# Performance work log

Hardware: AMD Instinct MI355X
Metric: run time of the kernel (lower is better)

Reference implementation:

```python
import jax, jax.numpy as jnp
import numpy as np
from jax import lax

NUM_STEPS = 32
NUM_CLASSES = 10
HIDDEN = 1024


def setup_inputs() -> dict:
    key = jax.random.key(0)
    ks = jax.random.split(key, 4)
    B, H, W, C = 8, 1024, 2048, 4
    x = jax.random.normal(ks[0], (B, H, W, C), dtype=jnp.float32)
    conv_w = jax.random.normal(ks[1], (C,), dtype=jnp.float32) * 0.5
    conv_b = jnp.zeros((1,), dtype=jnp.float32)
    w1 = jax.random.normal(ks[2], (HIDDEN, W), dtype=jnp.float32) * (1.0 / np.sqrt(W))
    b1 = jnp.zeros((HIDDEN,), dtype=jnp.float32)
    w2 = jax.random.normal(ks[3], (NUM_CLASSES, HIDDEN), dtype=jnp.float32) * (1.0 / np.sqrt(HIDDEN))
    b2 = jnp.zeros((NUM_CLASSES,), dtype=jnp.float32)
    beta1 = jnp.full((1,), 0.95, dtype=jnp.float32)
    thr1 = jnp.ones((1,), dtype=jnp.float32)
    beta2 = jnp.full((1,), 0.95, dtype=jnp.float32)
    thr2 = jnp.ones((1,), dtype=jnp.float32)
    return {"x": x, "conv_w": conv_w, "conv_b": conv_b, "w1": w1, "b1": b1,
            "beta1": beta1, "thr1": thr1, "w2": w2, "b2": b2,
            "beta2": beta2, "thr2": thr2}


def _leaky_scan(inp_t, beta, thr):
    # inp_t: [T, ...]; snntorch Leaky, reset_mechanism='subtract', reset_delay=False
    b = jnp.clip(beta, 0.0, 1.0)

    def step(mem, u):
        mem = b * mem + u
        spk = (mem > thr).astype(u.dtype)   # heaviside spike
        mem = mem - spk * thr               # subtract reset (no delay)
        return mem, spk

    mem0 = jnp.zeros(inp_t.shape[1:], dtype=inp_t.dtype)
    _, spks = lax.scan(step, mem0, inp_t)
    return spks  # [T, ...]


def reference(x, conv_w, conv_b, w1, b1, beta1, thr1, w2, b2, beta2, thr2):
    # x: [B, H, W, 4]; 1x1 conv over 4 antenna channels -> 1 channel
    xf = jnp.einsum('bhwc,c->bhw', x, conv_w) + conv_b[0]       # [B, H, W]
    B, H, W = xf.shape
    G = H // NUM_STEPS
    xr = xf.reshape(B, G, NUM_STEPS, W)                          # [B, G, T, 2048]
    h = jnp.einsum('bgtw,dw->bgtd', xr, w1) + b1                 # [B, G, T, D]
    spks1 = _leaky_scan(jnp.moveaxis(h, 2, 0), beta1, thr1)      # [T, B, G, D]
    s = spks1.sum(axis=0)                                        # [B, G, D]
    h2 = jnp.einsum('bgd,cd->bgc', s, w2) + b2                   # [B, G, C]
    spks2 = _leaky_scan(jnp.moveaxis(h2, 1, 0), beta2, thr2)     # [G, B, C]
    logits = spks2.sum(axis=0)                                   # [B, C]
    return jax.nn.softmax(logits, axis=1)
```

## Files before the change

kernel.cpp:

```cpp
#include <hip/hip_runtime.h>

#define TSTEPS 32
#define HID 1024
#define NCLS 10
#define BATCH 8
#define GGRP 32
#define MROWS 8192
#define GK 2048
#define GN 1024
#define BUFSH 16384
#define CLDS 40

typedef __attribute__((ext_vector_type(8))) short bf16x8;
typedef __attribute__((ext_vector_type(16))) float f32x16;

__device__ __forceinline__ unsigned short bf16_rne(float v) {
    unsigned u = __builtin_bit_cast(unsigned, v);
    return (unsigned short)((u + 0x7FFFu + ((u >> 16) & 1u)) >> 16);
}
__device__ __forceinline__ float bf16_f(unsigned short h) {
    unsigned u = (unsigned)h << 16;
    return __builtin_bit_cast(float, u);
}
__device__ __forceinline__ void gload16(const unsigned short* g, unsigned short* l) {
    __builtin_amdgcn_global_load_lds(
        (const __attribute__((address_space(1))) void*)g,
        (__attribute__((address_space(3))) void*)l, 16, 0, 0);
}


__global__ __launch_bounds__(256) void conv_pack_kernel(
    const float4* __restrict__ x, const float* __restrict__ cw,
    const float* __restrict__ cb,
    unsigned short* __restrict__ Ahi, unsigned short* __restrict__ Alo)
{
    __shared__ __align__(16) unsigned short lh[128 * CLDS];
    __shared__ __align__(16) unsigned short ll[128 * CLDS];
    const int rb = blockIdx.x >> 6;
    const int kb = blockIdx.x & 63;
    const float c0 = cw[0], c1 = cw[1], c2 = cw[2], c3 = cw[3], cbv = cb[0];
    const int tid = threadIdx.x;

#pragma unroll
    for (int p = 0; p < 16; ++p) {
        int i = p * 256 + tid;
        int row = i >> 5, px = i & 31;
        float4 a = x[(size_t)(rb * 128 + row) * 2048 + kb * 32 + px];
        float v = a.x * c0 + a.y * c1 + a.z * c2 + a.w * c3 + cbv;
        unsigned short h = bf16_rne(v);
        lh[row * CLDS + px] = h;
        ll[row * CLDS + px] = bf16_rne(v - bf16_f(h));
    }
    __syncthreads();

#pragma unroll
    for (int cc = 0; cc < 2; ++cc) {
        int c = tid + cc * 256;
        int u = c >> 6, w = c & 63;
        int row = (u >> 1) * 32 + (w & 31);
        int ko  = (u & 1) * 2 + (w >> 5);
        bf16x8 h8 = *(const bf16x8*)(lh + row * CLDS + ko * 8);
        bf16x8 l8 = *(const bf16x8*)(ll + row * CLDS + ko * 8);
        size_t off = ((size_t)blockIdx.x * 512 + c) * 8;
        *(bf16x8*)(Ahi + off) = h8;
        *(bf16x8*)(Alo + off) = l8;
    }
}

__global__ __launch_bounds__(256) void wpack_kernel(
    const float* __restrict__ wsrc, unsigned short* __restrict__ Bhi,
    unsigned short* __restrict__ Blo)
{
    const int kb  = blockIdx.x & 63;
    const int cbk = blockIdx.x >> 6;
    const int tid = threadIdx.x;
#pragma unroll
    for (int cc = 0; cc < 2; ++cc) {
        int c = tid + cc * 256;
        int u = c >> 6, w = c & 63;
        int row = (u >> 1) * 32 + (w & 31);
        int k0  = (u & 1) * 16 + (w >> 5) * 8;
        const float* pw = wsrc + ((size_t)(cbk * 128 + row) * 2048 + kb * 32 + k0);
        bf16x8 h8, l8;
#pragma unroll
        for (int e = 0; e < 8; ++e) {
            float v = pw[e];
            unsigned short h = bf16_rne(v);
            h8[e] = (short)h;
            l8[e] = (short)bf16_rne(v - bf16_f(h));
        }
        size_t off = ((size_t)blockIdx.x * 512 + c) * 8;
        *(bf16x8*)(Bhi + off) = h8;
        *(bf16x8*)(Blo + off) = l8;
    }
}

__global__ __launch_bounds__(256, 2) void gemm_scan_kernel(
    const unsigned short* __restrict__ Ahi, const unsigned short* __restrict__ Alo,
    const unsigned short* __restrict__ Bhi, const unsigned short* __restrict__ Blo,
    const float* __restrict__ bias,
    const float* __restrict__ beta1, const float* __restrict__ thr1,
    float* __restrict__ S)
{
    __shared__ __align__(16) unsigned short sm[2 * BUFSH];

    const int tid = threadIdx.x;
    const int lane = tid & 63, wv = tid >> 6;
    const int wr = wv >> 1, wc = wv & 1;
    const int by = blockIdx.x & 63;
    const int bx = blockIdx.x >> 6;

    const unsigned short* gAh = Ahi + (size_t)by * 262144;
    const unsigned short* gAl = Alo + (size_t)by * 262144;
    const unsigned short* gBh = Bhi + (size_t)bx * 262144;
    const unsigned short* gBl = Blo + (size_t)bx * 262144;

    f32x16 acc[2][2];
#pragma unroll
    for (int i = 0; i < 2; ++i)
#pragma unroll
        for (int j = 0; j < 2; ++j) acc[i][j] = (f32x16)0.f;

    bf16x8 fr[2][16];

#define STAGE(buf, kb_)                                                          \
    {                                                                            \
        unsigned short* dst = sm + (buf) * BUFSH + tid * 8;                      \
        const size_t o = (size_t)(kb_) * 4096 + tid * 8;                         \
        gload16(gAh + o, dst);                                                   \
        gload16(gAh + o + 2048, dst + 2048);                                     \
        gload16(gAl + o, dst + 4096);                                            \
        gload16(gAl + o + 2048, dst + 6144);                                     \
        gload16(gBh + o, dst + 8192);                                            \
        gload16(gBh + o + 2048, dst + 10240);                                    \
        gload16(gBl + o, dst + 12288);                                           \
        gload16(gBl + o + 2048, dst + 14336);                                    \
    }

#define READF(s, bufp)                                                           \
    {                                                                            \
        const unsigned short* bp_ = (bufp);                                      \
        _Pragma("unroll")                                                        \
        for (int i = 0; i < 2; ++i)                                              \
            _Pragma("unroll")                                                    \
            for (int kh = 0; kh < 2; ++kh) {                                     \
                int ua = ((wr * 2 + i) * 2 + kh) * 512 + fo;                     \
                fr[s][(i * 2 + kh) * 2 + 0] = *(const bf16x8*)(bp_ + ua);        \
                fr[s][(i * 2 + kh) * 2 + 1] = *(const bf16x8*)(bp_ + 4096 + ua); \
            }                                                                    \
        _Pragma("unroll")                                                        \
        for (int j = 0; j < 2; ++j)                                              \
            _Pragma("unroll")                                                    \
            for (int kh = 0; kh < 2; ++kh) {                                     \
                int ub = ((wc * 2 + j) * 2 + kh) * 512 + fo;                     \
                fr[s][8 + (j * 2 + kh) * 2 + 0] = *(const bf16x8*)(bp_ + 8192 + ub);  \
                fr[s][8 + (j * 2 + kh) * 2 + 1] = *(const bf16x8*)(bp_ + 12288 + ub); \
            }                                                                    \
    }

#define MFMAF(s)                                                                 \
    {                                                                            \
        _Pragma("unroll")                                                        \
        for (int kh = 0; kh < 2; ++kh) {                                         \
            _Pragma("unroll")                                                    \
            for (int i = 0; i < 2; ++i)                                          \
                _Pragma("unroll")                                                \
                for (int j = 0; j < 2; ++j)                                      \
                    acc[i][j] = __builtin_amdgcn_mfma_f32_32x32x16_bf16(         \
                        fr[s][(i * 2 + kh) * 2], fr[s][8 + (j * 2 + kh) * 2],    \
                        acc[i][j], 0, 0, 0);                                     \
            _Pragma("unroll")                                                    \
            for (int i = 0; i < 2; ++i)                                          \
                _Pragma("unroll")                                                \
                for (int j = 0; j < 2; ++j)                                      \
                    acc[i][j] = __builtin_amdgcn_mfma_f32_32x32x16_bf16(         \
                        fr[s][(i * 2 + kh) * 2], fr[s][8 + (j * 2 + kh) * 2 + 1],\
                        acc[i][j], 0, 0, 0);                                     \
            _Pragma("unroll")                                                    \
            for (int i = 0; i < 2; ++i)                                          \
                _Pragma("unroll")                                                \
                for (int j = 0; j < 2; ++j)                                      \
                    acc[i][j] = __builtin_amdgcn_mfma_f32_32x32x16_bf16(         \
                        fr[s][(i * 2 + kh) * 2 + 1], fr[s][8 + (j * 2 + kh) * 2],\
                        acc[i][j], 0, 0, 0);                                     \
        }                                                                        \
    }

#define KSTEP(SC, SN, KB, DOSTAGE)                                               \
    {                                                                            \
        asm volatile("s_waitcnt vmcnt(0)" ::: "memory");                         \
        asm volatile("s_waitcnt lgkmcnt(0)" ::: "memory");                       \
        __builtin_amdgcn_sched_barrier(0);                                       \
        __builtin_amdgcn_s_barrier();                                            \
        if (DOSTAGE) STAGE(((KB) + 1) & 1, (KB) + 1);                            \
        READF(SN, sm + ((KB) & 1) * BUFSH);                                      \
        MFMAF(SC);                                                               \
    }

    STAGE(0, 0);
    STAGE(1, 1);
    asm volatile("s_waitcnt vmcnt(8)" ::: "memory");
    __builtin_amdgcn_s_barrier();
    const int fo = ((lane & 31) + 32 * (lane >> 5)) * 8;
    READF(0, sm);

    for (int kb = 1; kb < 63; kb += 2) {
        KSTEP(0, 1, kb, 1);
        KSTEP(1, 0, kb + 1, 1);
    }
    KSTEP(0, 1, 63, 0);
    asm volatile("s_waitcnt lgkmcnt(0)" ::: "memory");
    __builtin_amdgcn_sched_barrier(0);
    MFMAF(1);
    __syncthreads();

    float* sb = (float*)sm;
    const float bclamp = fminf(fmaxf(beta1[0], 0.f), 1.f);
    const float th = thr1[0];

#pragma unroll
    for (int i = 0; i < 2; ++i)
#pragma unroll
        for (int j = 0; j < 2; ++j)
#pragma unroll
            for (int r = 0; r < 16; ++r) {
                int lr = wr * 64 + i * 32 + (r & 3) + 8 * (r >> 2) + 4 * (lane >> 5);
                int lc = wc * 64 + j * 32 + (lane & 31);
                sb[lr * 128 + lc] = acc[i][j][r];
            }
    __syncthreads();

    const int scol = tid & 127;
    const int half = tid >> 7;
    const float bv = bias[bx * 128 + scol];
#pragma unroll
    for (int p = 0; p < 2; ++p) {
        int gg = half * 2 + p;
        float mem = 0.f, cnt = 0.f;
#pragma unroll
        for (int t = 0; t < TSTEPS; ++t) {
            float u = sb[(gg * 32 + t) * 128 + scol] + bv;
            mem = bclamp * mem + u;
            float spk = mem > th ? 1.f : 0.f;
            mem -= spk * th;
            cnt += spk;
        }
        S[(size_t)(by * 4 + gg) * GN + bx * 128 + scol] = cnt;
    }
}

__global__ __launch_bounds__(256) void fc2_kernel(
    const float* __restrict__ s, const float* __restrict__ w2,
    const float* __restrict__ b2, float* __restrict__ h2)
{
    int bg  = blockIdx.x;
    int tid = threadIdx.x;
    const float* sp = s + (size_t)bg * HID;
    float part[NCLS];
#pragma unroll
    for (int c = 0; c < NCLS; ++c) part[c] = 0.f;
    for (int d = tid; d < HID; d += 256) {
        float sv = sp[d];
#pragma unroll
        for (int c = 0; c < NCLS; ++c) part[c] += sv * w2[c * HID + d];
    }
#pragma unroll
    for (int c = 0; c < NCLS; ++c)
        for (int off = 32; off > 0; off >>= 1)
            part[c] += __shfl_down(part[c], off, 64);
    __shared__ float red[NCLS][4];
    int wave = tid >> 6, lanei = tid & 63;
    if (lanei == 0)
#pragma unroll
        for (int c = 0; c < NCLS; ++c) red[c][wave] = part[c];
    __syncthreads();
    if (tid < NCLS) {
        float v = red[tid][0] + red[tid][1] + red[tid][2] + red[tid][3] + b2[tid];
        h2[bg * NCLS + tid] = v;
    }
}

__global__ __launch_bounds__(128) void scan2_kernel(
    const float* __restrict__ h2, const float* __restrict__ beta2,
    const float* __restrict__ thr2, float* __restrict__ out)
{
    __shared__ float logits[BATCH][NCLS];
    int t = threadIdx.x;
    if (t < BATCH * NCLS) {
        int b = t / NCLS, c = t % NCLS;
        float bb = fminf(fmaxf(beta2[0], 0.f), 1.f);
        float th = thr2[0];
        float mem = 0.f, lg = 0.f;
        for (int g = 0; g < GGRP; ++g) {
            float u = h2[(b * GGRP + g) * NCLS + c];
            mem = bb * mem + u;
            float spk = mem > th ? 1.f : 0.f;
            mem -= spk * th;
            lg += spk;
        }
        logits[b][c] = lg;
    }
    __syncthreads();
    if (t < BATCH) {
        float mx = -1e30f;
        for (int c = 0; c < NCLS; ++c) mx = fmaxf(mx, logits[t][c]);
        float e[NCLS];
        float sum = 0.f;
        for (int c = 0; c < NCLS; ++c) { e[c] = expf(logits[t][c] - mx); sum += e[c]; }
        for (int c = 0; c < NCLS; ++c) out[t * NCLS + c] = e[c] / sum;
    }
}

extern "C" void kernel_launch(void* const* d_in, const int* in_sizes, int n_in,
                              void* d_out, int out_size, void* d_ws, size_t ws_size,
                              hipStream_t stream)
{
    const float* x     = (const float*)d_in[0];
    const float* cw    = (const float*)d_in[1];
    const float* cb    = (const float*)d_in[2];
    const float* w1    = (const float*)d_in[3];
    const float* b1    = (const float*)d_in[4];
    const float* beta1 = (const float*)d_in[5];
    const float* thr1  = (const float*)d_in[6];
    const float* w2    = (const float*)d_in[7];
    const float* b2    = (const float*)d_in[8];
    const float* beta2 = (const float*)d_in[9];
    const float* thr2  = (const float*)d_in[10];
    float* out = (float*)d_out;

    unsigned short* ahi = (unsigned short*)d_ws;
    unsigned short* alo = ahi + (size_t)MROWS * GK;
    unsigned short* bhi = alo + (size_t)MROWS * GK;
    unsigned short* blo = bhi + (size_t)GN * GK;
    float* s  = (float*)(blo + (size_t)GN * GK);
    float* h2 = s + (size_t)BATCH * GGRP * HID;

    conv_pack_kernel<<<4096, 256, 0, stream>>>((const float4*)x, cw, cb, ahi, alo);
    wpack_kernel    <<<512, 256, 0, stream>>>(w1, bhi, blo);
    gemm_scan_kernel<<<512, 256, 0, stream>>>(ahi, alo, bhi, blo, b1, beta1, thr1, s);
    fc2_kernel      <<<256, 256, 0, stream>>>(s, w2, b2, h2);
    scan2_kernel    <<<1, 128, 0, stream>>>(h2, beta2, thr2, out);
}
```

Before: 163.3 us.

## Load B fragments directly from global into registers, bypassing LDS

Only the A operand (hi/lo split) is now staged through LDS. Each wave loads its B-operand fragments straight from global memory into registers, one k-block ahead, with relaxed vmcnt waits. This halves LDS traffic and staging per k-step and frees shared memory. The cost is more register pressure, exposed global-load latency on B, and a vmcnt accounting that is easy to get wrong. Since B was pre-laid out in fragment order, each lane's direct loads are contiguous.

```diff
diff --git a/kernel.cpp b/kernel.cpp
--- a/kernel.cpp
+++ b/kernel.cpp
@@ -8,7 +8,7 @@
 #define MROWS 8192
 #define GK 2048
 #define GN 1024
-#define BUFSH 16384
+#define ABUF 8192
 #define CLDS 40
 
 typedef __attribute__((ext_vector_type(8))) short bf16x8;
@@ -102,7 +102,7 @@
     const float* __restrict__ beta1, const float* __restrict__ thr1,
     float* __restrict__ S)
 {
-    __shared__ __align__(16) unsigned short sm[2 * BUFSH];
+    __shared__ __align__(16) unsigned short sm[32768];
 
     const int tid = threadIdx.x;
     const int lane = tid & 63, wv = tid >> 6;
@@ -112,8 +112,9 @@
 
     const unsigned short* gAh = Ahi + (size_t)by * 262144;
     const unsigned short* gAl = Alo + (size_t)by * 262144;
-    const unsigned short* gBh = Bhi + (size_t)bx * 262144;
-    const unsigned short* gBl = Blo + (size_t)bx * 262144;
+    const int fo = ((lane & 31) + 32 * (lane >> 5)) * 8;
+    const unsigned short* pBh = Bhi + (size_t)bx * 262144 + fo;
+    const unsigned short* pBl = Blo + (size_t)bx * 262144 + fo;
 
     f32x16 acc[2][2];
 #pragma unroll
@@ -123,21 +124,31 @@
 
     bf16x8 fr[2][16];
 
-#define STAGE(buf, kb_)                                                          \
-    {                                                                            \
-        unsigned short* dst = sm + (buf) * BUFSH + tid * 8;                      \
+#define STAGE_A(buf, kb_)                                                        \
+    {                                                                            \
+        unsigned short* dst = sm + (buf) * ABUF + tid * 8;                       \
         const size_t o = (size_t)(kb_) * 4096 + tid * 8;                         \
         gload16(gAh + o, dst);                                                   \
         gload16(gAh + o + 2048, dst + 2048);                                     \
         gload16(gAl + o, dst + 4096);                                            \
         gload16(gAl + o + 2048, dst + 6144);                                     \
-        gload16(gBh + o, dst + 8192);                                            \
-        gload16(gBh + o + 2048, dst + 10240);                                    \
-        gload16(gBl + o, dst + 12288);                                           \
-        gload16(gBl + o + 2048, dst + 14336);                                    \
-    }
-
-#define READF(s, bufp)                                                           \
+    }
+
+#define LOADB(s, kb_)                                                            \
+    {                                                                            \
+        const unsigned short* bh_ = pBh + (size_t)(kb_) * 4096;                  \
+        const unsigned short* bl_ = pBl + (size_t)(kb_) * 4096;                  \
+        _Pragma("unroll")                                                        \
+        for (int j = 0; j < 2; ++j)                                              \
+            _Pragma("unroll")                                                    \
+            for (int kh = 0; kh < 2; ++kh) {                                     \
+                int u = (wc * 2 + j) * 2 + kh;                                   \
+                fr[s][8 + (j * 2 + kh) * 2 + 0] = *(const bf16x8*)(bh_ + u * 512); \
+                fr[s][8 + (j * 2 + kh) * 2 + 1] = *(const bf16x8*)(bl_ + u * 512); \
+            }                                                                    \
+    }
+
+#define READFA(s, bufp)                                                          \
     {                                                                            \
         const unsigned short* bp_ = (bufp);                                      \
         _Pragma("unroll")                                                        \
@@ -147,14 +158,6 @@
                 int ua = ((wr * 2 + i) * 2 + kh) * 512 + fo;                     \
                 fr[s][(i * 2 + kh) * 2 + 0] = *(const bf16x8*)(bp_ + ua);        \
                 fr[s][(i * 2 + kh) * 2 + 1] = *(const bf16x8*)(bp_ + 4096 + ua); \
-            }                                                                    \
-        _Pragma("unroll")                                                        \
-        for (int j = 0; j < 2; ++j)                                              \
-            _Pragma("unroll")                                                    \
-            for (int kh = 0; kh < 2; ++kh) {                                     \
-                int ub = ((wc * 2 + j) * 2 + kh) * 512 + fo;                     \
-                fr[s][8 + (j * 2 + kh) * 2 + 0] = *(const bf16x8*)(bp_ + 8192 + ub);  \
-                fr[s][8 + (j * 2 + kh) * 2 + 1] = *(const bf16x8*)(bp_ + 12288 + ub); \
             }                                                                    \
     }
 
@@ -186,29 +189,35 @@
         }                                                                        \
     }
 
-#define KSTEP(SC, SN, KB, DOSTAGE)                                               \
-    {                                                                            \
-        asm volatile("s_waitcnt vmcnt(0)" ::: "memory");                         \
+#define KSTEP(SC, SN, KB, DOSTAGE, DOLOADB, VMC)                                 \
+    {                                                                            \
+        asm volatile("s_waitcnt vmcnt(" #VMC ")" ::: "memory");                  \
         asm volatile("s_waitcnt lgkmcnt(0)" ::: "memory");                       \
         __builtin_amdgcn_sched_barrier(0);                                       \
         __builtin_amdgcn_s_barrier();                                            \
-        if (DOSTAGE) STAGE(((KB) + 1) & 1, (KB) + 1);                            \
-        READF(SN, sm + ((KB) & 1) * BUFSH);                                      \
+        if (DOSTAGE) STAGE_A(((KB) + 1) & 1, (KB) + 1);                          \
+        READFA(SN, sm + ((KB) & 1) * ABUF);                                      \
         MFMAF(SC);                                                               \
-    }
-
-    STAGE(0, 0);
-    STAGE(1, 1);
-    asm volatile("s_waitcnt vmcnt(8)" ::: "memory");
+        if (DOLOADB) LOADB(SC, (KB) + 1);                                        \
+    }
+
+    LOADB(0, 0);
+    LOADB(1, 1);
+    STAGE_A(0, 0);
+    STAGE_A(1, 1);
+    asm volatile("s_waitcnt vmcnt(4)" ::: "memory");
     __builtin_amdgcn_s_barrier();
-    const int fo = ((lane & 31) + 32 * (lane >> 5)) * 8;
-    READF(0, sm);
-
-    for (int kb = 1; kb < 63; kb += 2) {
-        KSTEP(0, 1, kb, 1);
-        KSTEP(1, 0, kb + 1, 1);
-    }
-    KSTEP(0, 1, 63, 0);
+    READFA(0, sm);
+
+    KSTEP(0, 1, 1, 1, 1, 0);
+    KSTEP(1, 0, 2, 1, 1, 8);
+    for (int kb = 3; kb < 61; kb += 2) {
+        KSTEP(0, 1, kb, 1, 1, 8);
+        KSTEP(1, 0, kb + 1, 1, 1, 8);
+    }
+    KSTEP(0, 1, 61, 1, 1, 8);
+    KSTEP(1, 0, 62, 1, 1, 8);
+    KSTEP(0, 1, 63, 0, 0, 8);
     asm volatile("s_waitcnt lgkmcnt(0)" ::: "memory");
     __builtin_amdgcn_sched_barrier(0);
     MFMAF(1);
```

After: 167.2 us. 2.4% more time.
